# Kernel optimization log

Measured on AMD Instinct MI355X. Metric: run time of the kernel, lower is better.

## Reference

```python
import jax, jax.numpy as jnp
import numpy as np
import math

B, L, C, H = 2, 2048, 768, 12
D = C // H
MAX_SCALE_MUL = math.log(100.0)


def setup_inputs() -> dict:
    key = jax.random.key(0)
    ks = jax.random.split(key, 8)
    std = 0.02
    x = jax.random.normal(ks[0], (B, L, C), dtype=jnp.float32)
    attn_bias = jax.random.normal(ks[1], (1, 1, L, L), dtype=jnp.float32)
    W_qkv = jax.random.normal(ks[2], (3 * C, C), dtype=jnp.float32) * std
    b_qkv = jnp.zeros((3 * C,), dtype=jnp.float32)
    # attn_l2_norm=True: learned per-head log-scale, init log(4)
    scale_mul_log = jnp.full((1, H, 1, 1), math.log(4.0), dtype=jnp.float32)
    W_proj = jax.random.normal(ks[3], (C, C), dtype=jnp.float32) * std
    b_proj = jnp.zeros((C,), dtype=jnp.float32)
    return {"x": x, "attn_bias": attn_bias, "W_qkv": W_qkv, "b_qkv": b_qkv,
            "scale_mul_log": scale_mul_log, "W_proj": W_proj, "b_proj": b_proj}


def _l2norm(t):
    # matches F.normalize(dim=-1, eps=1e-12)
    n = jnp.sqrt(jnp.sum(t * t, axis=-1, keepdims=True))
    return t / jnp.maximum(n, 1e-12)


def reference(x, attn_bias, W_qkv, b_qkv, scale_mul_log, W_proj, b_proj):
    Bx, Lx, Cx = x.shape
    qkv = (x @ W_qkv.T + b_qkv).reshape(Bx, Lx, 3, H, D)
    # -> [3, B, H, L, D]
    qkv = jnp.transpose(qkv, (2, 0, 3, 1, 4))
    q, k, v = qkv[0], qkv[1], qkv[2]
    scale_mul = jnp.exp(jnp.minimum(scale_mul_log, MAX_SCALE_MUL))  # [1,H,1,1]
    q = _l2norm(q) * scale_mul
    k = _l2norm(k)
    # scale = 1 in the l2-norm branch
    attn = jnp.einsum('bhqd,bhkd->bhqk', q, k) + attn_bias
    attn = jax.nn.softmax(attn, axis=-1)
    oup = jnp.einsum('bhqk,bhkd->bhqd', attn, v)          # [B,H,L,D]
    oup = jnp.transpose(oup, (0, 2, 1, 3)).reshape(Bx, Lx, Cx)
    return oup @ W_proj.T + b_proj
```

## Files before the change

### kernel.cpp

```cpp
#include <hip/hip_runtime.h>
#include <math.h>

#define B_ 2
#define L_ 2048
#define C_ 768
#define H_ 12
#define D_ 64
#define M_ (B_ * L_)
#define MAXLOG 4.605170185988091f

typedef __bf16 bf16;
typedef __bf16 bf16x4 __attribute__((ext_vector_type(4)));
typedef __bf16 bf16x8 __attribute__((ext_vector_type(8)));
typedef float  f32x4  __attribute__((ext_vector_type(4)));

#define SZ_  ((size_t)B_ * H_ * L_ * D_)
#define MC_  ((size_t)M_ * C_)
#define WQ_  ((size_t)3 * C_ * C_)
#define WP_  ((size_t)C_ * C_)

__global__ __launch_bounds__(256) void prep(
    const float4* __restrict__ x, const float4* __restrict__ Wq,
    const float4* __restrict__ Wp,
    bf16* __restrict__ xb, bf16* __restrict__ wqb,
    bf16* __restrict__ Wh, bf16* __restrict__ Wl,
    float4* __restrict__ zbase)
{
    const int X4 = (int)(MC_ / 4);
    const int W4 = (int)(WQ_ / 4);
    const int S4 = (int)(WP_ / 4);
    const int Z4 = (int)((3 * SZ_ + 2 * MC_) * sizeof(bf16) / 16);
    const int total = X4 + W4 + S4 + Z4;

    const int i0 = blockIdx.x * 256 + threadIdx.x;
    const int stride = gridDim.x * 256;
    for (int i = i0; i < total; i += stride) {
        if (i < X4) {
            const float4 v = x[i];
            bf16x4 o; o[0]=(bf16)v.x; o[1]=(bf16)v.y; o[2]=(bf16)v.z; o[3]=(bf16)v.w;
            *(bf16x4*)&xb[(size_t)i * 4] = o;
        } else if (i < X4 + W4) {
            const int j = i - X4;
            const float4 v = Wq[j];
            bf16x4 o; o[0]=(bf16)v.x; o[1]=(bf16)v.y; o[2]=(bf16)v.z; o[3]=(bf16)v.w;
            *(bf16x4*)&wqb[(size_t)j * 4] = o;
        } else if (i < X4 + W4 + S4) {
            const int j = i - X4 - W4;
            const float4 v = Wp[j];
            bf16x4 h, l;
            h[0]=(bf16)v.x; l[0]=(bf16)(v.x-(float)h[0]);
            h[1]=(bf16)v.y; l[1]=(bf16)(v.y-(float)h[1]);
            h[2]=(bf16)v.z; l[2]=(bf16)(v.z-(float)h[2]);
            h[3]=(bf16)v.w; l[3]=(bf16)(v.w-(float)h[3]);
            *(bf16x4*)&Wh[(size_t)j * 4] = h;
            *(bf16x4*)&Wl[(size_t)j * 4] = l;
        } else {
            zbase[i - X4 - W4 - S4] = (float4){0.f, 0.f, 0.f, 0.f};
        }
    }
}

__global__ __launch_bounds__(256) void qkv_mfma(
    const bf16* __restrict__ A, const bf16* __restrict__ W,
    const float* __restrict__ bias, const float* __restrict__ sml,
    bf16* __restrict__ qb, bf16* __restrict__ kb, bf16* __restrict__ vtb)
{
    __shared__ __align__(16) bf16 As[128][72];
    __shared__ __align__(16) bf16 Bs[64][72];

    const int t    = threadIdx.x;
    const int w    = t >> 6;
    const int lane = t & 63;
    const int quad = lane >> 4;
    const int c    = lane & 15;
    const int m0   = blockIdx.x * 128;
    const int n0   = blockIdx.y * 64;

    f32x4 acc[2][4];
    #pragma unroll
    for (int mt = 0; mt < 2; ++mt)
        #pragma unroll
        for (int nt = 0; nt < 4; ++nt) acc[mt][nt] = (f32x4){0.f,0.f,0.f,0.f};

    for (int kt = 0; kt < C_; kt += 64) {
        __syncthreads();
        #pragma unroll
        for (int p = 0; p < 4; ++p) {
            const int idx = t + p * 256;
            const int row = idx >> 3;
            const int cg  = (idx & 7) * 8;
            *(bf16x8*)&As[row][cg] = *(const bf16x8*)&A[(size_t)(m0 + row) * C_ + kt + cg];
        }
        #pragma unroll
        for (int p = 0; p < 2; ++p) {
            const int idx = t + p * 256;
            const int row = idx >> 3;
            const int cg  = (idx & 7) * 8;
            *(bf16x8*)&Bs[row][cg] = *(const bf16x8*)&W[(size_t)(n0 + row) * C_ + kt + cg];
        }
        __syncthreads();

        #pragma unroll
        for (int ks = 0; ks < 2; ++ks) {
            #pragma unroll
            for (int mt = 0; mt < 2; ++mt) {
                const bf16x8 a = *(const bf16x8*)&As[w * 32 + mt * 16 + c][ks * 32 + quad * 8];
                #pragma unroll
                for (int nt = 0; nt < 4; ++nt) {
                    const bf16x8 b = *(const bf16x8*)&Bs[nt * 16 + c][ks * 32 + quad * 8];
                    acc[mt][nt] = __builtin_amdgcn_mfma_f32_16x16x32_bf16(a, b, acc[mt][nt], 0, 0, 0);
                }
            }
        }
    }

    const int three = blockIdx.y / H_;
    const int h     = blockIdx.y % H_;
    const int bidx  = m0 >> 11;
    const int l0    = (m0 & (L_ - 1)) + w * 32;

    if (three < 2) {
        bf16* dst = (three == 0) ? qb : kb;
        const float scale = (three == 0) ? expf(fminf(sml[h], MAXLOG)) : 1.0f;
        #pragma unroll
        for (int mt = 0; mt < 2; ++mt) {
            float val[4][4];
            float ss[4] = {0.f, 0.f, 0.f, 0.f};
            #pragma unroll
            for (int nt = 0; nt < 4; ++nt) {
                const float bb = bias[n0 + nt * 16 + c];
                #pragma unroll
                for (int reg = 0; reg < 4; ++reg) {
                    const float v = acc[mt][nt][reg] + bb;
                    val[nt][reg] = v;
                    ss[reg] += v * v;
                }
            }
            #pragma unroll
            for (int reg = 0; reg < 4; ++reg) {
                float s = ss[reg];
                #pragma unroll
                for (int off = 1; off < 16; off <<= 1) s += __shfl_xor(s, off, 16);
                const float inv = scale / fmaxf(sqrtf(s), 1e-12f);
                const int l = l0 + mt * 16 + quad * 4 + reg;
                #pragma unroll
                for (int nt = 0; nt < 4; ++nt)
                    dst[((size_t)(bidx * H_ + h) * L_ + l) * D_ + nt * 16 + c] =
                        (bf16)(val[nt][reg] * inv);
            }
        }
    } else {
        #pragma unroll
        for (int mt = 0; mt < 2; ++mt)
            #pragma unroll
            for (int nt = 0; nt < 4; ++nt) {
                const int d = nt * 16 + c;
                const float bb = bias[n0 + d];
                const int l = l0 + mt * 16 + quad * 4;
                bf16x4 o;
                #pragma unroll
                for (int reg = 0; reg < 4; ++reg) o[reg] = (bf16)(acc[mt][nt][reg] + bb);
                *(bf16x4*)&vtb[((size_t)(bidx * H_ + h) * D_ + d) * L_ + l] = o;
            }
    }
}

__global__ __launch_bounds__(256) void flash_mfma(
    const bf16* __restrict__ q, const bf16* __restrict__ k,
    const bf16* __restrict__ vt, const float* __restrict__ bias,
    const float* __restrict__ sml,
    bf16* __restrict__ aoh, bf16* __restrict__ aol)
{
    __shared__ __align__(16) bf16 QPs[64][72];
    __shared__ __align__(16) bf16 Ks [64][72];
    __shared__ __align__(16) bf16 Vts[64][72];

    const int t    = threadIdx.x;
    const int w    = t >> 6;
    const int lane = t & 63;
    const int quad = lane >> 4;
    const int c    = lane & 15;
    const int q0   = blockIdx.x * 64;
    const int bh   = blockIdx.y;
    const int h    = bh % H_;
    const int b    = bh / H_;
    const size_t base  = (size_t)bh * L_ * D_;
    const size_t vbase = (size_t)bh * D_ * L_;

    const float FMAX = expf(fminf(sml[h], MAXLOG)) + 8.0f;

    #pragma unroll
    for (int p = 0; p < 2; ++p) {
        const int f = t + p * 256;
        const int r = f >> 3, d0 = (f & 7) * 8;
        *(bf16x8*)&QPs[r][d0] = *(const bf16x8*)&q[base + (size_t)(q0 + r) * D_ + d0];
    }
    __syncthreads();
    bf16x8 Qreg[2];
    Qreg[0] = *(const bf16x8*)&QPs[w * 16 + c][quad * 8];
    Qreg[1] = *(const bf16x8*)&QPs[w * 16 + c][32 + quad * 8];

    const int rbase = q0 + w * 16 + quad * 4;

    const int r0  = t >> 3,        c00 = (t & 7) * 8;
    const int r1  = (t + 256) >> 3, c01 = ((t + 256) & 7) * 8;

    bf16x8 kreg[2], vreg[2];
    float  breg[4][4];
    kreg[0] = *(const bf16x8*)&k [base  + (size_t)r0 * D_ + c00];
    kreg[1] = *(const bf16x8*)&k [base  + (size_t)r1 * D_ + c01];
    vreg[0] = *(const bf16x8*)&vt[vbase + (size_t)r0 * L_ + c00];
    vreg[1] = *(const bf16x8*)&vt[vbase + (size_t)r1 * L_ + c01];
    #pragma unroll
    for (int tile = 0; tile < 4; ++tile)
        #pragma unroll
        for (int reg = 0; reg < 4; ++reg)
            breg[tile][reg] = bias[(size_t)(rbase + reg) * L_ + tile * 16 + c];

    float l_acc[4] = {0.f, 0.f, 0.f, 0.f};
    f32x4 O[4];
    #pragma unroll
    for (int i = 0; i < 4; ++i) O[i] = (f32x4){0.f, 0.f, 0.f, 0.f};

    for (int kt = 0; kt < L_; kt += 64) {
        __syncthreads();

        *(bf16x8*)&Ks [r0][c00] = kreg[0];
        *(bf16x8*)&Ks [r1][c01] = kreg[1];
        *(bf16x8*)&Vts[r0][c00] = vreg[0];
        *(bf16x8*)&Vts[r1][c01] = vreg[1];

        f32x4 S[4];
        #pragma unroll
        for (int tile = 0; tile < 4; ++tile)
            #pragma unroll
            for (int reg = 0; reg < 4; ++reg)
                S[tile][reg] = breg[tile][reg];

        const int kt2 = kt + 64;
        if (kt2 < L_) {
            kreg[0] = *(const bf16x8*)&k [base  + (size_t)(kt2 + r0) * D_ + c00];
            kreg[1] = *(const bf16x8*)&k [base  + (size_t)(kt2 + r1) * D_ + c01];
            vreg[0] = *(const bf16x8*)&vt[vbase + (size_t)r0 * L_ + kt2 + c00];
            vreg[1] = *(const bf16x8*)&vt[vbase + (size_t)r1 * L_ + kt2 + c01];
            #pragma unroll
            for (int tile = 0; tile < 4; ++tile)
                #pragma unroll
                for (int reg = 0; reg < 4; ++reg)
                    breg[tile][reg] = bias[(size_t)(rbase + reg) * L_ + kt2 + tile * 16 + c];
        }
        __syncthreads();

        #pragma unroll
        for (int ks = 0; ks < 2; ++ks) {
            #pragma unroll
            for (int tile = 0; tile < 4; ++tile) {
                const bf16x8 bb = *(const bf16x8*)&Ks[tile * 16 + c][ks * 32 + quad * 8];
                S[tile] = __builtin_amdgcn_mfma_f32_16x16x32_bf16(Qreg[ks], bb, S[tile], 0, 0, 0);
            }
        }

        #pragma unroll
        for (int tile = 0; tile < 4; ++tile)
            #pragma unroll
            for (int reg = 0; reg < 4; ++reg) {
                const float pv = __expf(S[tile][reg] - FMAX);
                l_acc[reg] += pv;
                QPs[w * 16 + quad * 4 + reg][tile * 16 + c] = (bf16)pv;
            }
        __syncthreads();

        #pragma unroll
        for (int ks = 0; ks < 2; ++ks) {
            const bf16x8 a = *(const bf16x8*)&QPs[w * 16 + c][ks * 32 + quad * 8];
            #pragma unroll
            for (int tile = 0; tile < 4; ++tile) {
                const bf16x8 bb = *(const bf16x8*)&Vts[tile * 16 + c][ks * 32 + quad * 8];
                O[tile] = __builtin_amdgcn_mfma_f32_16x16x32_bf16(a, bb, O[tile], 0, 0, 0);
            }
        }
    }

    #pragma unroll
    for (int reg = 0; reg < 4; ++reg) {
        float rs = l_acc[reg];
        #pragma unroll
        for (int off = 1; off < 16; off <<= 1) rs += __shfl_xor(rs, off, 16);
        const float linv = 1.0f / rs;
        const int   row  = q0 + w * 16 + quad * 4 + reg;
        const size_t o   = ((size_t)(b * L_ + row)) * C_ + h * 64 + c;
        #pragma unroll
        for (int tile = 0; tile < 4; ++tile) {
            const float v  = O[tile][reg] * linv;
            const bf16  hv = (bf16)v;
            aoh[o + tile * 16] = hv;
            aol[o + tile * 16] = (bf16)(v - (float)hv);
        }
    }
}

__global__ __launch_bounds__(256) void proj_mfma(
    const bf16* __restrict__ Ahg, const bf16* __restrict__ Alg,
    const bf16* __restrict__ Whg, const bf16* __restrict__ Wlg,
    const float* __restrict__ bias, float* __restrict__ outp)
{
    __shared__ __align__(16) bf16 Ah[128][72];
    __shared__ __align__(16) bf16 Al[128][72];
    __shared__ __align__(16) bf16 Bh[64][72];
    __shared__ __align__(16) bf16 Bl[64][72];

    const int t    = threadIdx.x;
    const int w    = t >> 6;
    const int lane = t & 63;
    const int quad = lane >> 4;
    const int c    = lane & 15;
    const int m0   = blockIdx.x * 128;
    const int n0   = blockIdx.y * 64;

    f32x4 acc[2][4];
    #pragma unroll
    for (int mt = 0; mt < 2; ++mt)
        #pragma unroll
        for (int nt = 0; nt < 4; ++nt) acc[mt][nt] = (f32x4){0.f,0.f,0.f,0.f};

    for (int kt = 0; kt < C_; kt += 64) {
        __syncthreads();
        #pragma unroll
        for (int p = 0; p < 4; ++p) {
            const int idx = t + p * 256;
            const int row = idx >> 3;
            const int cg  = (idx & 7) * 8;
            *(bf16x8*)&Ah[row][cg] = *(const bf16x8*)&Ahg[(size_t)(m0 + row) * C_ + kt + cg];
            *(bf16x8*)&Al[row][cg] = *(const bf16x8*)&Alg[(size_t)(m0 + row) * C_ + kt + cg];
        }
        #pragma unroll
        for (int p = 0; p < 2; ++p) {
            const int idx = t + p * 256;
            const int row = idx >> 3;
            const int cg  = (idx & 7) * 8;
            *(bf16x8*)&Bh[row][cg] = *(const bf16x8*)&Whg[(size_t)(n0 + row) * C_ + kt + cg];
            *(bf16x8*)&Bl[row][cg] = *(const bf16x8*)&Wlg[(size_t)(n0 + row) * C_ + kt + cg];
        }
        __syncthreads();

        #pragma unroll
        for (int ks = 0; ks < 2; ++ks) {
            #pragma unroll
            for (int mt = 0; mt < 2; ++mt) {
                const bf16x8 ah = *(const bf16x8*)&Ah[w * 32 + mt * 16 + c][ks * 32 + quad * 8];
                const bf16x8 al = *(const bf16x8*)&Al[w * 32 + mt * 16 + c][ks * 32 + quad * 8];
                #pragma unroll
                for (int nt = 0; nt < 4; ++nt) {
                    const bf16x8 bh = *(const bf16x8*)&Bh[nt * 16 + c][ks * 32 + quad * 8];
                    const bf16x8 bl = *(const bf16x8*)&Bl[nt * 16 + c][ks * 32 + quad * 8];
                    acc[mt][nt] = __builtin_amdgcn_mfma_f32_16x16x32_bf16(ah, bh, acc[mt][nt], 0, 0, 0);
                    acc[mt][nt] = __builtin_amdgcn_mfma_f32_16x16x32_bf16(ah, bl, acc[mt][nt], 0, 0, 0);
                    acc[mt][nt] = __builtin_amdgcn_mfma_f32_16x16x32_bf16(al, bh, acc[mt][nt], 0, 0, 0);
                }
            }
        }
    }

    #pragma unroll
    for (int mt = 0; mt < 2; ++mt)
        #pragma unroll
        for (int nt = 0; nt < 4; ++nt) {
            const int col = n0 + nt * 16 + c;
            const float bb = bias[col];
            #pragma unroll
            for (int reg = 0; reg < 4; ++reg) {
                const int row = m0 + w * 32 + mt * 16 + quad * 4 + reg;
                outp[(size_t)row * C_ + col] = acc[mt][nt][reg] + bb;
            }
        }
}

extern "C" void kernel_launch(void* const* d_in, const int* in_sizes, int n_in,
                              void* d_out, int out_size, void* d_ws, size_t ws_size,
                              hipStream_t stream)
{
    const float* x         = (const float*)d_in[0];
    const float* attn_bias = (const float*)d_in[1];
    const float* W_qkv     = (const float*)d_in[2];
    const float* b_qkv     = (const float*)d_in[3];
    const float* sml       = (const float*)d_in[4];
    const float* W_proj    = (const float*)d_in[5];
    const float* b_proj    = (const float*)d_in[6];
    float* out = (float*)d_out;

    bf16* qb  = (bf16*)d_ws;
    bf16* kb  = qb  + SZ_;
    bf16* vtb = kb  + SZ_;
    bf16* aoh = vtb + SZ_;
    bf16* aol = aoh + MC_;
    bf16* Wh  = aol + MC_;
    bf16* Wl  = Wh  + WP_;
    bf16* xb  = Wl  + WP_;
    bf16* wqb = xb  + MC_;

    prep<<<2048, 256, 0, stream>>>(
        (const float4*)x, (const float4*)W_qkv, (const float4*)W_proj,
        xb, wqb, Wh, Wl, (float4*)qb);

    qkv_mfma<<<dim3(M_ / 128, (3 * C_) / 64), 256, 0, stream>>>(
        xb, wqb, b_qkv, sml, qb, kb, vtb);

    flash_mfma<<<dim3(L_ / 64, B_ * H_), 256, 0, stream>>>(
        qb, kb, vtb, attn_bias, sml, aoh, aol);

    proj_mfma<<<dim3(M_ / 128, C_ / 64), 256, 0, stream>>>(
        aoh, aol, Wh, Wl, b_proj, out);
}
```

Measured before the change: 209.4 us.

## Register-prefetch next K tile in QKV and proj GEMMs; shrink proj M tile

Both GEMM kernels now load the next 64-wide K slice from global memory into registers while the current slice is being consumed from shared memory, so global latency overlaps with MFMA work. The projection kernel also drops from 128-row to 64-row tiles, doubling its grid (384 to 768 blocks) to fill more CUs on the small M=4096, N=768 problem. In exchange, more registers are held for the prefetch, and the smaller proj tiles re-read the weights more often.

```diff
diff --git a/kernel.cpp b/kernel.cpp
--- a/kernel.cpp
+++ b/kernel.cpp
@@ -76,27 +76,38 @@
     const int m0   = blockIdx.x * 128;
     const int n0   = blockIdx.y * 64;
 
+    const int r0 = t >> 3;
+    const int cg = (t & 7) * 8;
+
     f32x4 acc[2][4];
     #pragma unroll
     for (int mt = 0; mt < 2; ++mt)
         #pragma unroll
         for (int nt = 0; nt < 4; ++nt) acc[mt][nt] = (f32x4){0.f,0.f,0.f,0.f};
 
+    bf16x8 areg[4], breg[2];
+    #pragma unroll
+    for (int p = 0; p < 4; ++p)
+        areg[p] = *(const bf16x8*)&A[(size_t)(m0 + r0 + 32 * p) * C_ + cg];
+    #pragma unroll
+    for (int p = 0; p < 2; ++p)
+        breg[p] = *(const bf16x8*)&W[(size_t)(n0 + r0 + 32 * p) * C_ + cg];
+
     for (int kt = 0; kt < C_; kt += 64) {
         __syncthreads();
         #pragma unroll
-        for (int p = 0; p < 4; ++p) {
-            const int idx = t + p * 256;
-            const int row = idx >> 3;
-            const int cg  = (idx & 7) * 8;
-            *(bf16x8*)&As[row][cg] = *(const bf16x8*)&A[(size_t)(m0 + row) * C_ + kt + cg];
-        }
-        #pragma unroll
-        for (int p = 0; p < 2; ++p) {
-            const int idx = t + p * 256;
-            const int row = idx >> 3;
-            const int cg  = (idx & 7) * 8;
-            *(bf16x8*)&Bs[row][cg] = *(const bf16x8*)&W[(size_t)(n0 + row) * C_ + kt + cg];
+        for (int p = 0; p < 4; ++p) *(bf16x8*)&As[r0 + 32 * p][cg] = areg[p];
+        #pragma unroll
+        for (int p = 0; p < 2; ++p) *(bf16x8*)&Bs[r0 + 32 * p][cg] = breg[p];
+
+        const int kt2 = kt + 64;
+        if (kt2 < C_) {
+            #pragma unroll
+            for (int p = 0; p < 4; ++p)
+                areg[p] = *(const bf16x8*)&A[(size_t)(m0 + r0 + 32 * p) * C_ + kt2 + cg];
+            #pragma unroll
+            for (int p = 0; p < 2; ++p)
+                breg[p] = *(const bf16x8*)&W[(size_t)(n0 + r0 + 32 * p) * C_ + kt2 + cg];
         }
         __syncthreads();
 
@@ -202,7 +213,7 @@
 
     const int rbase = q0 + w * 16 + quad * 4;
 
-    const int r0  = t >> 3,        c00 = (t & 7) * 8;
+    const int r0  = t >> 3,         c00 = (t & 7) * 8;
     const int r1  = (t + 256) >> 3, c01 = ((t + 256) & 7) * 8;
 
     bf16x8 kreg[2], vreg[2];
@@ -304,8 +315,8 @@
     const bf16* __restrict__ Whg, const bf16* __restrict__ Wlg,
     const float* __restrict__ bias, float* __restrict__ outp)
 {
-    __shared__ __align__(16) bf16 Ah[128][72];
-    __shared__ __align__(16) bf16 Al[128][72];
+    __shared__ __align__(16) bf16 Ah[64][72];
+    __shared__ __align__(16) bf16 Al[64][72];
     __shared__ __align__(16) bf16 Bh[64][72];
     __shared__ __align__(16) bf16 Bl[64][72];
 
@@ -314,65 +325,72 @@
     const int lane = t & 63;
     const int quad = lane >> 4;
     const int c    = lane & 15;
-    const int m0   = blockIdx.x * 128;
+    const int m0   = blockIdx.x * 64;
     const int n0   = blockIdx.y * 64;
 
-    f32x4 acc[2][4];
-    #pragma unroll
-    for (int mt = 0; mt < 2; ++mt)
-        #pragma unroll
-        for (int nt = 0; nt < 4; ++nt) acc[mt][nt] = (f32x4){0.f,0.f,0.f,0.f};
+    const int r0 = t >> 3;
+    const int cg = (t & 7) * 8;
+
+    f32x4 acc[4];
+    #pragma unroll
+    for (int nt = 0; nt < 4; ++nt) acc[nt] = (f32x4){0.f,0.f,0.f,0.f};
+
+    bf16x8 ahreg[2], alreg[2], bhreg[2], blreg[2];
+    #pragma unroll
+    for (int p = 0; p < 2; ++p) {
+        ahreg[p] = *(const bf16x8*)&Ahg[(size_t)(m0 + r0 + 32 * p) * C_ + cg];
+        alreg[p] = *(const bf16x8*)&Alg[(size_t)(m0 + r0 + 32 * p) * C_ + cg];
+        bhreg[p] = *(const bf16x8*)&Whg[(size_t)(n0 + r0 + 32 * p) * C_ + cg];
+        blreg[p] = *(const bf16x8*)&Wlg[(size_t)(n0 + r0 + 32 * p) * C_ + cg];
+    }
 
     for (int kt = 0; kt < C_; kt += 64) {
         __syncthreads();
         #pragma unroll
-        for (int p = 0; p < 4; ++p) {
-            const int idx = t + p * 256;
-            const int row = idx >> 3;
-            const int cg  = (idx & 7) * 8;
-            *(bf16x8*)&Ah[row][cg] = *(const bf16x8*)&Ahg[(size_t)(m0 + row) * C_ + kt + cg];
-            *(bf16x8*)&Al[row][cg] = *(const bf16x8*)&Alg[(size_t)(m0 + row) * C_ + kt + cg];
-        }
-        #pragma unroll
         for (int p = 0; p < 2; ++p) {
-            const int idx = t + p * 256;
-            const int row = idx >> 3;
-            const int cg  = (idx & 7) * 8;
-            *(bf16x8*)&Bh[row][cg] = *(const bf16x8*)&Whg[(size_t)(n0 + row) * C_ + kt + cg];
-            *(bf16x8*)&Bl[row][cg] = *(const bf16x8*)&Wlg[(size_t)(n0 + row) * C_ + kt + cg];
+            *(bf16x8*)&Ah[r0 + 32 * p][cg] = ahreg[p];
+            *(bf16x8*)&Al[r0 + 32 * p][cg] = alreg[p];
+            *(bf16x8*)&Bh[r0 + 32 * p][cg] = bhreg[p];
+            *(bf16x8*)&Bl[r0 + 32 * p][cg] = blreg[p];
+        }
+
+        const int kt2 = kt + 64;
+        if (kt2 < C_) {
+            #pragma unroll
+            for (int p = 0; p < 2; ++p) {
+                ahreg[p] = *(const bf16x8*)&Ahg[(size_t)(m0 + r0 + 32 * p) * C_ + kt2 + cg];
+                alreg[p] = *(const bf16x8*)&Alg[(size_t)(m0 + r0 + 32 * p) * C_ + kt2 + cg];
+                bhreg[p] = *(const bf16x8*)&Whg[(size_t)(n0 + r0 + 32 * p) * C_ + kt2 + cg];
+                blreg[p] = *(const bf16x8*)&Wlg[(size_t)(n0 + r0 + 32 * p) * C_ + kt2 + cg];
+            }
         }
         __syncthreads();
 
         #pragma unroll
         for (int ks = 0; ks < 2; ++ks) {
-            #pragma unroll
-            for (int mt = 0; mt < 2; ++mt) {
-                const bf16x8 ah = *(const bf16x8*)&Ah[w * 32 + mt * 16 + c][ks * 32 + quad * 8];
-                const bf16x8 al = *(const bf16x8*)&Al[w * 32 + mt * 16 + c][ks * 32 + quad * 8];
-                #pragma unroll
-                for (int nt = 0; nt < 4; ++nt) {
-                    const bf16x8 bh = *(const bf16x8*)&Bh[nt * 16 + c][ks * 32 + quad * 8];
-                    const bf16x8 bl = *(const bf16x8*)&Bl[nt * 16 + c][ks * 32 + quad * 8];
-                    acc[mt][nt] = __builtin_amdgcn_mfma_f32_16x16x32_bf16(ah, bh, acc[mt][nt], 0, 0, 0);
-                    acc[mt][nt] = __builtin_amdgcn_mfma_f32_16x16x32_bf16(ah, bl, acc[mt][nt], 0, 0, 0);
-                    acc[mt][nt] = __builtin_amdgcn_mfma_f32_16x16x32_bf16(al, bh, acc[mt][nt], 0, 0, 0);
-                }
-            }
-        }
-    }
-
-    #pragma unroll
-    for (int mt = 0; mt < 2; ++mt)
-        #pragma unroll
-        for (int nt = 0; nt < 4; ++nt) {
-            const int col = n0 + nt * 16 + c;
-            const float bb = bias[col];
-            #pragma unroll
-            for (int reg = 0; reg < 4; ++reg) {
-                const int row = m0 + w * 32 + mt * 16 + quad * 4 + reg;
-                outp[(size_t)row * C_ + col] = acc[mt][nt][reg] + bb;
-            }
-        }
+            const bf16x8 ah = *(const bf16x8*)&Ah[w * 16 + c][ks * 32 + quad * 8];
+            const bf16x8 al = *(const bf16x8*)&Al[w * 16 + c][ks * 32 + quad * 8];
+            #pragma unroll
+            for (int nt = 0; nt < 4; ++nt) {
+                const bf16x8 bh = *(const bf16x8*)&Bh[nt * 16 + c][ks * 32 + quad * 8];
+                const bf16x8 bl = *(const bf16x8*)&Bl[nt * 16 + c][ks * 32 + quad * 8];
+                acc[nt] = __builtin_amdgcn_mfma_f32_16x16x32_bf16(ah, bh, acc[nt], 0, 0, 0);
+                acc[nt] = __builtin_amdgcn_mfma_f32_16x16x32_bf16(ah, bl, acc[nt], 0, 0, 0);
+                acc[nt] = __builtin_amdgcn_mfma_f32_16x16x32_bf16(al, bh, acc[nt], 0, 0, 0);
+            }
+        }
+    }
+
+    #pragma unroll
+    for (int nt = 0; nt < 4; ++nt) {
+        const int col = n0 + nt * 16 + c;
+        const float bb = bias[col];
+        #pragma unroll
+        for (int reg = 0; reg < 4; ++reg) {
+            const int row = m0 + w * 16 + quad * 4 + reg;
+            outp[(size_t)row * C_ + col] = acc[nt][reg] + bb;
+        }
+    }
 }
 
 extern "C" void kernel_launch(void* const* d_in, const int* in_sizes, int n_in,
@@ -408,6 +426,6 @@
     flash_mfma<<<dim3(L_ / 64, B_ * H_), 256, 0, stream>>>(
         qb, kb, vtb, attn_bias, sml, aoh, aol);
 
-    proj_mfma<<<dim3(M_ / 128, C_ / 64), 256, 0, stream>>>(
+    proj_mfma<<<dim3(M_ / 64, C_ / 64), 256, 0, stream>>>(
         aoh, aol, Wh, Wl, b_proj, out);
 }
```

Result: no change. 206.2 us (-1.5%).
